# Kernel tuning notes

Hardware: AMD Instinct MI355X
Metric: run time of the kernel (lower is better)

## Reference

```python
import jax, jax.numpy as jnp
import numpy as np

B, N, C, H = 8, 1024, 768, 12
D = C // H
SCALE = D ** -0.5
BN_EPS = 1e-5


def setup_inputs() -> dict:
    key = jax.random.key(0)
    ks = jax.random.split(key, 8)
    s = 0.02
    return {
        "x": jax.random.normal(ks[0], (B, N, C), dtype=jnp.float32),
        "w_qkv": jax.random.normal(ks[1], (3 * C, C), dtype=jnp.float32) * s,
        "b_qkv": jnp.zeros((3 * C,), dtype=jnp.float32),
        "w_re": jax.random.normal(ks[2], (H, H), dtype=jnp.float32) * (1.0 / np.sqrt(H)),
        "b_re": jnp.zeros((H,), dtype=jnp.float32),
        "bn_gamma": jnp.ones((H,), dtype=jnp.float32),
        "bn_beta": jnp.zeros((H,), dtype=jnp.float32),
        "w_proj": jax.random.normal(ks[3], (C, C), dtype=jnp.float32) * s,
        "b_proj": jnp.zeros((C,), dtype=jnp.float32),
    }


def reference(x, w_qkv, b_qkv, w_re, b_re, bn_gamma, bn_beta, w_proj, b_proj):
    # qkv projection: (B,N,3C) -> (3,B,H,N,D)
    qkv = (x @ w_qkv.T + b_qkv).reshape(B, N, 3, H, D).transpose(2, 0, 3, 1, 4)
    q, k, v = qkv[0], qkv[1], qkv[2]
    # scaled dot-product attention scores, full [B,H,N,N] materialized (as in source)
    attn = jax.nn.softmax(jnp.einsum('bhnd,bhmd->bhnm', q, k) * SCALE, axis=-1)
    # 1x1 conv mixing heads: out[g] = sum_h w_re[g,h] * attn[h] + b_re[g]
    attn = jnp.einsum('bhnm,gh->bgnm', attn, w_re) + b_re[None, :, None, None]
    # BatchNorm2d over channels=heads (training-mode batch stats, biased var)
    mean = jnp.mean(attn, axis=(0, 2, 3), keepdims=True)
    var = jnp.var(attn, axis=(0, 2, 3), keepdims=True)
    attn = (attn - mean) / jnp.sqrt(var + BN_EPS)
    attn = attn * bn_gamma[None, :, None, None] + bn_beta[None, :, None, None]
    # reatten_scale = 1.0 (transform_scale=False)
    out = jnp.einsum('bhnm,bhmd->bhnd', attn, v)  # (B,H,N,D)
    out = out.transpose(0, 2, 1, 3).reshape(B, N, C)
    out = out @ w_proj.T + b_proj
    return out, attn
```

## Files before the change

### kernel.cpp

```cpp
#include <hip/hip_runtime.h>
#include <hip/hip_bf16.h>


typedef __attribute__((ext_vector_type(8))) short s16x8;
typedef __attribute__((ext_vector_type(4))) float f32x4;

#define QK_SCALE 0.18033688011112042f

__device__ __forceinline__ f32x4 mfma16(s16x8 a, s16x8 b, f32x4 c) {
    return __builtin_amdgcn_mfma_f32_16x16x32_bf16(a, b, c, 0, 0, 0);
}

__device__ __forceinline__ unsigned short f2bf(float f) {
    unsigned u = __float_as_uint(f);
    u += 0x7fffu + ((u >> 16) & 1u);
    return (unsigned short)(u >> 16);
}

__global__ __launch_bounds__(256) void cvt_bf16_k(const float* __restrict__ in,
                                                  unsigned short* __restrict__ out, int n4) {
    int i = blockIdx.x * 256 + threadIdx.x;
    if (i < n4) {
        float4 v = ((const float4*)in)[i];
        ushort4 o;
        o.x = f2bf(v.x); o.y = f2bf(v.y); o.z = f2bf(v.z); o.w = f2bf(v.w);
        ((ushort4*)out)[i] = o;
    }
}

__global__ __launch_bounds__(256) void gemm_qkv_k(
    const unsigned short* __restrict__ A,
    const unsigned short* __restrict__ Bw,
    const float* __restrict__ bias,
    unsigned short* __restrict__ qs, unsigned short* __restrict__ ks,
    unsigned short* __restrict__ vs)
{
    __shared__ unsigned short Al[128 * 32];
    __shared__ unsigned short Bl[128 * 32];
    const int tid = threadIdx.x, wv = tid >> 6, ln = tid & 63;
    const int r = ln & 15, q = ln >> 4;
    const int i0 = blockIdx.y * 128, j0 = blockIdx.x * 128;
    const int wm = (wv & 1) * 64, wn = (wv >> 1) * 64;
    const int srow = tid >> 2, scol = (tid & 3) * 8;
    f32x4 acc[4][4] = {};
    for (int kb = 0; kb < 768; kb += 32) {
        s16x8 av0 = *(const s16x8*)(A  + (size_t)(i0 + srow) * 768 + kb + scol);
        s16x8 av1 = *(const s16x8*)(A  + (size_t)(i0 + srow + 64) * 768 + kb + scol);
        s16x8 bv0 = *(const s16x8*)(Bw + (size_t)(j0 + srow) * 768 + kb + scol);
        s16x8 bv1 = *(const s16x8*)(Bw + (size_t)(j0 + srow + 64) * 768 + kb + scol);
        __syncthreads();
        *(s16x8*)(Al + srow * 32 + scol)        = av0;
        *(s16x8*)(Al + (srow + 64) * 32 + scol) = av1;
        *(s16x8*)(Bl + srow * 32 + scol)        = bv0;
        *(s16x8*)(Bl + (srow + 64) * 32 + scol) = bv1;
        __syncthreads();
        s16x8 af[4], bf[4];
#pragma unroll
        for (int mt = 0; mt < 4; mt++) af[mt] = *(const s16x8*)(Al + (wm + mt * 16 + r) * 32 + q * 8);
#pragma unroll
        for (int nt = 0; nt < 4; nt++) bf[nt] = *(const s16x8*)(Bl + (wn + nt * 16 + r) * 32 + q * 8);
#pragma unroll
        for (int mt = 0; mt < 4; mt++)
#pragma unroll
            for (int nt = 0; nt < 4; nt++)
                acc[mt][nt] = mfma16(af[mt], bf[nt], acc[mt][nt]);
    }
#pragma unroll
    for (int nt = 0; nt < 4; nt++) {
        int j = j0 + wn + nt * 16 + r;
        int t = (j >= 1536) ? 2 : (j >= 768 ? 1 : 0);
        int rem = j - t * 768;
        int h = rem >> 6, d = rem & 63;
        float bb = bias[j];
#pragma unroll
        for (int mt = 0; mt < 4; mt++) {
#pragma unroll
            for (int rr = 0; rr < 4; rr++) {
                int i = i0 + wm + mt * 16 + q * 4 + rr;
                int bidx = i >> 10, n = i & 1023;
                float val = acc[mt][nt][rr] + bb;
                size_t off = (((size_t)bidx * 12 + h) * 1024 + n) * 64 + d;
                if (t == 0)      qs[off] = f2bf(val * QK_SCALE);
                else if (t == 1) ks[off] = f2bf(val);
                else             vs[off] = f2bf(val);
            }
        }
    }
}

__global__ __launch_bounds__(256) void transpose_v_k(const unsigned short* __restrict__ vs,
                                                     unsigned short* __restrict__ vT)
{
    __shared__ unsigned short t[64][65];
    const int tid = threadIdx.x;
    const int bh = blockIdx.x;
    const int n0 = blockIdx.y * 64;
    const unsigned short* src = vs + ((size_t)bh * 1024 + n0) * 64;
#pragma unroll
    for (int i = 0; i < 4; i++) {
        int id4 = tid + i * 256;
        int row = id4 >> 4, c4 = (id4 & 15) * 4;
        ushort4 v = *(const ushort4*)(src + row * 64 + c4);
        t[row][c4 + 0] = v.x; t[row][c4 + 1] = v.y; t[row][c4 + 2] = v.z; t[row][c4 + 3] = v.w;
    }
    __syncthreads();
#pragma unroll
    for (int i = 0; i < 4; i++) {
        int id4 = tid + i * 256;
        int d = id4 >> 4, c4 = (id4 & 15) * 4;
        ushort4 o;
        o.x = t[c4 + 0][d]; o.y = t[c4 + 1][d]; o.z = t[c4 + 2][d]; o.w = t[c4 + 3][d];
        *(ushort4*)(vT + ((size_t)bh * 64 + d) * 1024 + n0 + c4) = o;
    }
}

__global__ __launch_bounds__(256) void attn_stats_k(
    const unsigned short* __restrict__ qs, const unsigned short* __restrict__ ks,
    float* __restrict__ Lbuf, float* __restrict__ Cmat)
{
    __shared__ unsigned short P[16][520];
    const int tid = threadIdx.x, wv = tid >> 6, ln = tid & 63;
    const int r = ln & 15, q = ln >> 4;
    const int b = blockIdx.x >> 6, n0 = (blockIdx.x & 63) * 16;
    const size_t bh0 = (size_t)b * 12;

    for (int i = tid; i < 16 * 520; i += 256) ((unsigned short*)P)[i] = 0;

    s16x8 qf[3][2];
#pragma unroll
    for (int hh = 0; hh < 3; hh++) {
        int h = wv * 3 + hh;
        const unsigned short* qp = qs + ((bh0 + h) * 1024 + n0 + r) * 64 + q * 8;
        qf[hh][0] = *(const s16x8*)qp;
        qf[hh][1] = *(const s16x8*)(qp + 32);
    }
    float rsum[3][4] = {};
    for (int m0 = 0; m0 < 1024; m0 += 32) {
#pragma unroll
        for (int hh = 0; hh < 3; hh++) {
            int h = wv * 3 + hh;
            const unsigned short* kp = ks + (bh0 + h) * 1024 * 64;
            f32x4 sc0 = {0,0,0,0}, sc1 = {0,0,0,0};
#pragma unroll
            for (int s = 0; s < 2; s++) {
                s16x8 k0 = *(const s16x8*)(kp + (size_t)(m0 + r) * 64 + s * 32 + q * 8);
                s16x8 k1 = *(const s16x8*)(kp + (size_t)(m0 + 16 + r) * 64 + s * 32 + q * 8);
                sc0 = mfma16(qf[hh][s], k0, sc0);
                sc1 = mfma16(qf[hh][s], k1, sc1);
            }
#pragma unroll
            for (int rr = 0; rr < 4; rr++) {
                float v = exp2f(sc0[rr]) + exp2f(sc1[rr]);
#pragma unroll
                for (int msk = 8; msk; msk >>= 1) v += __shfl_xor(v, msk, 16);
                rsum[hh][rr] += v;
            }
        }
    }
    float invl[3][4];
#pragma unroll
    for (int hh = 0; hh < 3; hh++)
#pragma unroll
        for (int rr = 0; rr < 4; rr++) {
            invl[hh][rr] = 1.0f / rsum[hh][rr];
            if (r == 0) Lbuf[(bh0 + wv * 3 + hh) * 1024 + n0 + q * 4 + rr] = invl[hh][rr];
        }
    __syncthreads();
    f32x4 cacc = {0,0,0,0};
    for (int m0 = 0; m0 < 1024; m0 += 32) {
#pragma unroll
        for (int hh = 0; hh < 3; hh++) {
            int h = wv * 3 + hh;
            const unsigned short* kp = ks + (bh0 + h) * 1024 * 64;
            f32x4 sc0 = {0,0,0,0}, sc1 = {0,0,0,0};
#pragma unroll
            for (int s = 0; s < 2; s++) {
                s16x8 k0 = *(const s16x8*)(kp + (size_t)(m0 + r) * 64 + s * 32 + q * 8);
                s16x8 k1 = *(const s16x8*)(kp + (size_t)(m0 + 16 + r) * 64 + s * 32 + q * 8);
                sc0 = mfma16(qf[hh][s], k0, sc0);
                sc1 = mfma16(qf[hh][s], k1, sc1);
            }
#pragma unroll
            for (int rr = 0; rr < 4; rr++) {
                P[h][(q * 4 + rr) * 32 + r]      = f2bf(exp2f(sc0[rr]) * invl[hh][rr]);
                P[h][(q * 4 + rr) * 32 + 16 + r] = f2bf(exp2f(sc1[rr]) * invl[hh][rr]);
            }
        }
        __syncthreads();
#pragma unroll
        for (int kk = 0; kk < 4; kk++) {
            s16x8 pf = *(const s16x8*)(&P[r][wv * 128 + kk * 32 + q * 8]);
            cacc = mfma16(pf, pf, cacc);
        }
        __syncthreads();
    }
#pragma unroll
    for (int rr = 0; rr < 4; rr++)
        atomicAdd(&Cmat[(q * 4 + rr) * 16 + r], cacc[rr]);
}

__global__ void bn_stats_k(const float* __restrict__ Cmat,
                           const float* __restrict__ w_re, const float* __restrict__ b_re,
                           const float* __restrict__ gamma, const float* __restrict__ beta,
                           unsigned short* __restrict__ W2, float* __restrict__ c2)
{
    __shared__ float Cs[12][12];
    int tid = threadIdx.x;
    if (tid < 144) Cs[tid / 12][tid % 12] = Cmat[(tid / 12) * 16 + (tid % 12)];
    __syncthreads();
    if (tid < 16) {
        for (int hc = 0; hc < 32; hc++) W2[tid * 32 + hc] = 0;
        if (tid >= 12) c2[tid] = 0.f;
    }
    if (tid < 12) {
        const float S1 = 8192.f;
        const float cnt = 8388608.f;
        float wg[12];
        for (int h = 0; h < 12; h++) wg[h] = w_re[tid * 12 + h];
        float bg = b_re[tid];
        float sw = 0.f;
        for (int h = 0; h < 12; h++) sw += wg[h];
        float mean = sw * (S1 / cnt) + bg;
        float q2 = 0.f;
        for (int h = 0; h < 12; h++)
            for (int h2 = 0; h2 < 12; h2++) q2 += wg[h] * wg[h2] * Cs[h][h2];
        float sumsq = q2 + 2.f * bg * sw * S1 + cnt * bg * bg;
        float var = sumsq / cnt - mean * mean;
        float scale = gamma[tid] * rsqrtf(var + 1e-5f);
        c2[tid] = beta[tid] - mean * scale + scale * bg;
        for (int h = 0; h < 12; h++) W2[tid * 32 + h] = f2bf(scale * wg[h]);
    }
}

__global__ __launch_bounds__(256) void attn_out_k(
    const unsigned short* __restrict__ qs, const unsigned short* __restrict__ ks,
    const unsigned short* __restrict__ vT, const float* __restrict__ Lbuf,
    const unsigned short* __restrict__ W2, const float* __restrict__ c2,
    float* __restrict__ attnO, unsigned short* __restrict__ oh)
{
    __shared__ unsigned short P[512][32];
    __shared__ unsigned short AT[12][16][40];
    const int tid = threadIdx.x, wv = tid >> 6, ln = tid & 63;
    const int r = ln & 15, q = ln >> 4;
    const int b = blockIdx.x >> 6, n0 = (blockIdx.x & 63) * 16;
    const size_t bh0 = (size_t)b * 12;

    for (int i = tid; i < 512 * 32; i += 256) ((unsigned short*)P)[i] = 0;

    s16x8 qf[3][2];
    float invl[3][4];
#pragma unroll
    for (int hh = 0; hh < 3; hh++) {
        int h = wv * 3 + hh;
        const unsigned short* qp = qs + ((bh0 + h) * 1024 + n0 + r) * 64 + q * 8;
        qf[hh][0] = *(const s16x8*)qp;
        qf[hh][1] = *(const s16x8*)(qp + 32);
#pragma unroll
        for (int rr = 0; rr < 4; rr++)
            invl[hh][rr] = Lbuf[(bh0 + h) * 1024 + n0 + q * 4 + rr];
    }
    s16x8 w2f = *(const s16x8*)(W2 + r * 32 + q * 8);
    float c2v[4];
#pragma unroll
    for (int rr = 0; rr < 4; rr++) c2v[rr] = c2[q * 4 + rr];
    f32x4 pv[3][4] = {};
    __syncthreads();

    for (int m0 = 0; m0 < 1024; m0 += 32) {
#pragma unroll
        for (int hh = 0; hh < 3; hh++) {
            int h = wv * 3 + hh;
            const unsigned short* kp = ks + (bh0 + h) * 1024 * 64;
            f32x4 sc0 = {0,0,0,0}, sc1 = {0,0,0,0};
#pragma unroll
            for (int s = 0; s < 2; s++) {
                s16x8 k0 = *(const s16x8*)(kp + (size_t)(m0 + r) * 64 + s * 32 + q * 8);
                s16x8 k1 = *(const s16x8*)(kp + (size_t)(m0 + 16 + r) * 64 + s * 32 + q * 8);
                sc0 = mfma16(qf[hh][s], k0, sc0);
                sc1 = mfma16(qf[hh][s], k1, sc1);
            }
            int hb = h >> 3, hl = h & 7;
#pragma unroll
            for (int rr = 0; rr < 4; rr++) {
                int pt0 = (q * 4 + rr) * 32 + r;
                int pt1 = pt0 + 16;
                P[pt0][((hb + pt0) & 3) * 8 + hl] = f2bf(exp2f(sc0[rr]) * invl[hh][rr]);
                P[pt1][((hb + pt1) & 3) * 8 + hl] = f2bf(exp2f(sc1[rr]) * invl[hh][rr]);
            }
        }
        __syncthreads();
#pragma unroll
        for (int t = 0; t < 8; t++) {
            int pt = wv * 128 + t * 16 + r;
            s16x8 pf = *(const s16x8*)(&P[pt][((q + pt) & 3) * 8]);
            f32x4 d = mfma16(w2f, pf, f32x4{0, 0, 0, 0});
            int n = pt >> 5, m = pt & 31;
#pragma unroll
            for (int rr = 0; rr < 4; rr++) {
                int g = q * 4 + rr;
                if (g < 12) {
                    float av = d[rr] + c2v[rr];
                    attnO[((bh0 + g) * 1024 + n0 + n) * 1024 + m0 + m] = av;
                    AT[g][n][m] = f2bf(av);
                }
            }
        }
        __syncthreads();
#pragma unroll
        for (int hh = 0; hh < 3; hh++) {
            int g = wv * 3 + hh;
            s16x8 af = *(const s16x8*)(&AT[g][r][q * 8]);
            const unsigned short* vp = vT + (bh0 + g) * 64 * 1024;
#pragma unroll
            for (int dt = 0; dt < 4; dt++) {
                s16x8 vf = *(const s16x8*)(vp + (size_t)(dt * 16 + r) * 1024 + m0 + q * 8);
                pv[hh][dt] = mfma16(af, vf, pv[hh][dt]);
            }
        }
        __syncthreads();
    }
#pragma unroll
    for (int hh = 0; hh < 3; hh++) {
        int h = wv * 3 + hh;
#pragma unroll
        for (int dt = 0; dt < 4; dt++) {
#pragma unroll
            for (int rr = 0; rr < 4; rr++) {
                int n = n0 + q * 4 + rr;
                oh[((size_t)b * 1024 + n) * 768 + h * 64 + dt * 16 + r] = f2bf(pv[hh][dt][rr]);
            }
        }
    }
}

__global__ __launch_bounds__(256) void gemm_proj_k(
    const unsigned short* __restrict__ A,
    const unsigned short* __restrict__ Bw,
    const float* __restrict__ bias, float* __restrict__ Co)
{
    __shared__ unsigned short Al[128 * 32];
    __shared__ unsigned short Bl[128 * 32];
    const int tid = threadIdx.x, wv = tid >> 6, ln = tid & 63;
    const int r = ln & 15, q = ln >> 4;
    const int i0 = blockIdx.y * 128, j0 = blockIdx.x * 128;
    const int wm = (wv & 1) * 64, wn = (wv >> 1) * 64;
    const int srow = tid >> 2, scol = (tid & 3) * 8;
    f32x4 acc[4][4] = {};
    for (int kb = 0; kb < 768; kb += 32) {
        s16x8 av0 = *(const s16x8*)(A  + (size_t)(i0 + srow) * 768 + kb + scol);
        s16x8 av1 = *(const s16x8*)(A  + (size_t)(i0 + srow + 64) * 768 + kb + scol);
        s16x8 bv0 = *(const s16x8*)(Bw + (size_t)(j0 + srow) * 768 + kb + scol);
        s16x8 bv1 = *(const s16x8*)(Bw + (size_t)(j0 + srow + 64) * 768 + kb + scol);
        __syncthreads();
        *(s16x8*)(Al + srow * 32 + scol)        = av0;
        *(s16x8*)(Al + (srow + 64) * 32 + scol) = av1;
        *(s16x8*)(Bl + srow * 32 + scol)        = bv0;
        *(s16x8*)(Bl + (srow + 64) * 32 + scol) = bv1;
        __syncthreads();
        s16x8 af[4], bf[4];
#pragma unroll
        for (int mt = 0; mt < 4; mt++) af[mt] = *(const s16x8*)(Al + (wm + mt * 16 + r) * 32 + q * 8);
#pragma unroll
        for (int nt = 0; nt < 4; nt++) bf[nt] = *(const s16x8*)(Bl + (wn + nt * 16 + r) * 32 + q * 8);
#pragma unroll
        for (int mt = 0; mt < 4; mt++)
#pragma unroll
            for (int nt = 0; nt < 4; nt++)
                acc[mt][nt] = mfma16(af[mt], bf[nt], acc[mt][nt]);
    }
#pragma unroll
    for (int nt = 0; nt < 4; nt++) {
        int j = j0 + wn + nt * 16 + r;
        float bb = bias[j];
#pragma unroll
        for (int mt = 0; mt < 4; mt++) {
#pragma unroll
            for (int rr = 0; rr < 4; rr++) {
                int i = i0 + wm + mt * 16 + q * 4 + rr;
                Co[(size_t)i * 768 + j] = acc[mt][nt][rr] + bb;
            }
        }
    }
}

extern "C" void kernel_launch(void* const* d_in, const int* in_sizes, int n_in,
                              void* d_out, int out_size, void* d_ws, size_t ws_size,
                              hipStream_t stream)
{
    const float* x      = (const float*)d_in[0];
    const float* w_qkv  = (const float*)d_in[1];
    const float* b_qkv  = (const float*)d_in[2];
    const float* w_re   = (const float*)d_in[3];
    const float* b_re   = (const float*)d_in[4];
    const float* gamma  = (const float*)d_in[5];
    const float* beta   = (const float*)d_in[6];
    const float* w_proj = (const float*)d_in[7];
    const float* b_proj = (const float*)d_in[8];

    float* outp  = (float*)d_out;
    float* attnp = outp + 6291456;

    char* ws = (char*)d_ws;
    unsigned short* xb  = (unsigned short*)(ws);
    unsigned short* wqb = (unsigned short*)(ws + 12582912);
    unsigned short* wpb = (unsigned short*)(ws + 16121856);
    unsigned short* qs  = (unsigned short*)(ws + 17301504);
    unsigned short* ks  = (unsigned short*)(ws + 29884416);
    unsigned short* vs  = (unsigned short*)(ws + 42467328);
    unsigned short* vT  = (unsigned short*)(ws + 55050240);
    float* Lbuf         = (float*)(ws + 67633152);
    float* Cmat         = (float*)(ws + 68026368);
    unsigned short* W2  = (unsigned short*)(ws + 68027392);
    float* c2           = (float*)(ws + 68028416);
    unsigned short* oh  = xb;

    hipMemsetAsync(Cmat, 0, 1024, stream);
    cvt_bf16_k<<<6144, 256, 0, stream>>>(x,      xb,  1572864);
    cvt_bf16_k<<<1728, 256, 0, stream>>>(w_qkv,  wqb, 442368);
    cvt_bf16_k<<<576,  256, 0, stream>>>(w_proj, wpb, 147456);
    gemm_qkv_k<<<dim3(18, 64), 256, 0, stream>>>(xb, wqb, b_qkv, qs, ks, vs);
    transpose_v_k<<<dim3(96, 16), 256, 0, stream>>>(vs, vT);
    attn_stats_k<<<512, 256, 0, stream>>>(qs, ks, Lbuf, Cmat);
    bn_stats_k<<<1, 256, 0, stream>>>(Cmat, w_re, b_re, gamma, beta, W2, c2);
    attn_out_k<<<512, 256, 0, stream>>>(qs, ks, vT, Lbuf, W2, c2, attnp, oh);
    gemm_proj_k<<<dim3(6, 64), 256, 0, stream>>>(oh, wpb, b_proj, outp);
}
```

Before: 976.7 us.

## Fuse softmax-sum and head Gram passes in attention stats via unnormalized exponentials

The stats kernel previously made two full passes over K: one to compute softmax row sums and a second to recompute scores and build the head-by-head Gram matrix of normalized probabilities. It now makes a single pass. Unnormalized exponentials go to shared memory, and a per-row 16x16 Gram matrix is accumulated from them with MFMA. The row normalizers are applied afterwards as an outer-product scaling. This halves the QK^T MFMA and exp work and the K reads. In exchange it adds per-row MFMAs, a shared-memory reduction before the global atomics, and bf16 rounding of unnormalized exponentials, which could shift precision slightly.

```diff
diff --git a/kernel.cpp b/kernel.cpp
--- a/kernel.cpp
+++ b/kernel.cpp
@@ -118,13 +118,17 @@
     const unsigned short* __restrict__ qs, const unsigned short* __restrict__ ks,
     float* __restrict__ Lbuf, float* __restrict__ Cmat)
 {
-    __shared__ unsigned short P[16][520];
+    __shared__ unsigned short Et[16 * 546];
+    __shared__ float invLt[16][17];
+    __shared__ float Cred[256];
     const int tid = threadIdx.x, wv = tid >> 6, ln = tid & 63;
     const int r = ln & 15, q = ln >> 4;
     const int b = blockIdx.x >> 6, n0 = (blockIdx.x & 63) * 16;
     const size_t bh0 = (size_t)b * 12;
 
-    for (int i = tid; i < 16 * 520; i += 256) ((unsigned short*)P)[i] = 0;
+    for (int i = tid; i < 16 * 546; i += 256) Et[i] = 0;
+    for (int i = tid; i < 272; i += 256) (&invLt[0][0])[i] = 0.f;
+    Cred[tid] = 0.f;
 
     s16x8 qf[3][2];
 #pragma unroll
@@ -135,11 +139,14 @@
         qf[hh][1] = *(const s16x8*)(qp + 32);
     }
     float rsum[3][4] = {};
+    f32x4 Macc[4] = {};
+    __syncthreads();
+
     for (int m0 = 0; m0 < 1024; m0 += 32) {
 #pragma unroll
         for (int hh = 0; hh < 3; hh++) {
             int h = wv * 3 + hh;
-            const unsigned short* kp = ks + (bh0 + h) * 1024 * 64;
+            const unsigned short* kp = ks + (bh0 + h) * 65536;
             f32x4 sc0 = {0,0,0,0}, sc1 = {0,0,0,0};
 #pragma unroll
             for (int s = 0; s < 2; s++) {
@@ -150,53 +157,49 @@
             }
 #pragma unroll
             for (int rr = 0; rr < 4; rr++) {
-                float v = exp2f(sc0[rr]) + exp2f(sc1[rr]);
-#pragma unroll
-                for (int msk = 8; msk; msk >>= 1) v += __shfl_xor(v, msk, 16);
-                rsum[hh][rr] += v;
-            }
-        }
-    }
-    float invl[3][4];
+                float e0 = exp2f(sc0[rr]), e1 = exp2f(sc1[rr]);
+                rsum[hh][rr] += e0 + e1;
+                int base = (q * 4 + rr) * 546 + h * 34;
+                Et[base + r]      = f2bf(e0);
+                Et[base + 16 + r] = f2bf(e1);
+            }
+        }
+        __syncthreads();
+#pragma unroll
+        for (int t = 0; t < 4; t++) {
+            s16x8 ef = *(const s16x8*)(Et + (wv * 4 + t) * 546 + r * 34 + q * 8);
+            Macc[t] = mfma16(ef, ef, Macc[t]);
+        }
+        __syncthreads();
+    }
 #pragma unroll
     for (int hh = 0; hh < 3; hh++)
 #pragma unroll
         for (int rr = 0; rr < 4; rr++) {
-            invl[hh][rr] = 1.0f / rsum[hh][rr];
-            if (r == 0) Lbuf[(bh0 + wv * 3 + hh) * 1024 + n0 + q * 4 + rr] = invl[hh][rr];
-        }
-    __syncthreads();
-    f32x4 cacc = {0,0,0,0};
-    for (int m0 = 0; m0 < 1024; m0 += 32) {
-#pragma unroll
-        for (int hh = 0; hh < 3; hh++) {
-            int h = wv * 3 + hh;
-            const unsigned short* kp = ks + (bh0 + h) * 1024 * 64;
-            f32x4 sc0 = {0,0,0,0}, sc1 = {0,0,0,0};
-#pragma unroll
-            for (int s = 0; s < 2; s++) {
-                s16x8 k0 = *(const s16x8*)(kp + (size_t)(m0 + r) * 64 + s * 32 + q * 8);
-                s16x8 k1 = *(const s16x8*)(kp + (size_t)(m0 + 16 + r) * 64 + s * 32 + q * 8);
-                sc0 = mfma16(qf[hh][s], k0, sc0);
-                sc1 = mfma16(qf[hh][s], k1, sc1);
-            }
-#pragma unroll
-            for (int rr = 0; rr < 4; rr++) {
-                P[h][(q * 4 + rr) * 32 + r]      = f2bf(exp2f(sc0[rr]) * invl[hh][rr]);
-                P[h][(q * 4 + rr) * 32 + 16 + r] = f2bf(exp2f(sc1[rr]) * invl[hh][rr]);
-            }
-        }
-        __syncthreads();
-#pragma unroll
-        for (int kk = 0; kk < 4; kk++) {
-            s16x8 pf = *(const s16x8*)(&P[r][wv * 128 + kk * 32 + q * 8]);
-            cacc = mfma16(pf, pf, cacc);
-        }
-        __syncthreads();
+            float v = rsum[hh][rr];
+#pragma unroll
+            for (int msk = 8; msk; msk >>= 1) v += __shfl_xor(v, msk, 16);
+            float iv = 1.0f / v;
+            if (r == 0) {
+                Lbuf[(bh0 + wv * 3 + hh) * 1024 + n0 + q * 4 + rr] = iv;
+                invLt[q * 4 + rr][wv * 3 + hh] = iv;
+            }
+        }
+    __syncthreads();
+    float cl[4] = {0.f, 0.f, 0.f, 0.f};
+#pragma unroll
+    for (int t = 0; t < 4; t++) {
+        int n = wv * 4 + t;
+        float ih = invLt[n][r];
+#pragma unroll
+        for (int rr = 0; rr < 4; rr++)
+            cl[rr] += invLt[n][q * 4 + rr] * ih * Macc[t][rr];
     }
 #pragma unroll
     for (int rr = 0; rr < 4; rr++)
-        atomicAdd(&Cmat[(q * 4 + rr) * 16 + r], cacc[rr]);
+        atomicAdd(&Cred[(q * 4 + rr) * 16 + r], cl[rr]);
+    __syncthreads();
+    if (Cred[tid] != 0.f) atomicAdd(&Cmat[tid], Cred[tid]);
 }
 
 __global__ void bn_stats_k(const float* __restrict__ Cmat,
```

Result: faster. 862.6 us (-11.7%).
